# Kernel optimization log

Measured on AMD Instinct MI355X. Metric: run time of the kernel, lower is better.

Reference implementation:

```python
import jax, jax.numpy as jnp
import numpy as np

EPS = 1e-8


def _vb_layer(m, v, W_mu, W_var, relu_out, num_RF):
    """Variational linear layer with moment propagation.
    m: [N, in], v: [N, in] or None. W_mu/W_var: [out, in].
    """
    out_m = m @ W_mu.T
    m2 = m * m
    if v is None:
        out_v = m2 @ W_var.T
    else:
        out_v = (v + m2) @ W_var.T + v @ (W_mu * W_mu).T
    if relu_out:
        # random-feature ReLU output, scaled by sqrt(2/num_RF)
        scale = (2.0 / float(num_RF)) ** 0.5
        mask = (out_m > 0).astype(out_m.dtype)
        out_m = scale * jnp.maximum(out_m, 0.0)
        out_v = (scale * scale) * out_v * mask
    return out_m, out_v


def setup_inputs() -> dict:
    key = jax.random.key(0)
    ks = jax.random.split(key, 6)
    N, D0, R, D1, U = 262144, 128, 256, 64, 50000
    X = jax.random.normal(ks[0], (N, D0), dtype=jnp.float32)
    X_idx = jax.random.randint(ks[1], (N,), 0, U)
    W1_mu = jax.random.normal(ks[2], (R, D0), dtype=jnp.float32) / np.float32(np.sqrt(D0))
    W1_var = jax.random.uniform(ks[3], (R, D0), dtype=jnp.float32) * 0.1 + 0.01
    W2_mu = jax.random.normal(ks[4], (D1, R), dtype=jnp.float32) / np.float32(np.sqrt(R))
    W2_var = jax.random.uniform(ks[5], (D1, R), dtype=jnp.float32) * 0.1 + 0.01
    return {"X": X, "X_idx": X_idx, "W1_mu": W1_mu, "W1_var": W1_var,
            "W2_mu": W2_mu, "W2_var": W2_var, "num_unique": U}


def reference(X, X_idx, W1_mu, W1_var, W2_mu, W2_var, num_unique):
    num_RF = W1_mu.shape[0]
    # DGP layers: RF layer (ReLU features) then variational linear
    m, v = _vb_layer(X, None, W1_mu, W1_var, True, num_RF)
    m, v = _vb_layer(m, v, W2_mu, W2_var, False, num_RF)
    # precision-weighted segment reduction over X_idx
    precision = 1.0 / (v + EPS)          # [N, D1]
    weighted = precision * m             # [N, D1]
    p_sum = jax.ops.segment_sum(precision, X_idx, num_segments=num_unique) + EPS
    m_sum = jax.ops.segment_sum(weighted, X_idx, num_segments=num_unique)
    embedd_vars = 1.0 / p_sum            # [U, D1]
    embedd_means = m_sum * embedd_vars   # [U, D1]
    return embedd_means, embedd_vars
```

## Files before the change

kernel.cpp:

```cpp
#include <hip/hip_runtime.h>

#define EPSF 1e-8f

constexpr int D0 = 128;
constexpr int R  = 256;
constexpr int D1 = 64;
constexpr int BM = 64;
constexpr int NT = 512;
constexpr int TP = 68;

typedef __attribute__((ext_vector_type(8))) short  bf16x8;
typedef __attribute__((ext_vector_type(4))) float  f32x4;
typedef __attribute__((ext_vector_type(4))) uint   u32x4;

constexpr int WS_W1VAR = 32768;
constexpr int WS_W2MU  = 65536;
constexpr int WS_W2C   = 81920;
constexpr int WS_W2VAR = 98304;

__device__ __forceinline__ ushort f2bf(float x) {
    uint32_t u = __builtin_bit_cast(uint32_t, x);
    u += 0x7FFFu + ((u >> 16) & 1u);
    return (ushort)(u >> 16);
}

__device__ __forceinline__ uint cvt_pk_bf16(float lo, float hi) {
    uint r;
    asm("v_cvt_pk_bf16_f32 %0, %1, %2" : "=v"(r) : "v"(lo), "v"(hi));
    return r;
}

__device__ __forceinline__ bf16x8 sq_bf16x8(bf16x8 a) {
    u32x4 u = __builtin_bit_cast(u32x4, a);
    u32x4 r;
    #pragma unroll
    for (int i = 0; i < 4; ++i) {
        float lo = __builtin_bit_cast(float, u[i] << 16);
        float hi = __builtin_bit_cast(float, u[i] & 0xFFFF0000u);
        r[i] = cvt_pk_bf16(lo * lo, hi * hi);
    }
    return __builtin_bit_cast(bf16x8, r);
}

__global__ void convert_w(const float* __restrict__ W1mu,
                          const float* __restrict__ W1var,
                          const float* __restrict__ W2mu,
                          const float* __restrict__ W2var,
                          ushort* __restrict__ ws)
{
    int tid = blockIdx.x * 256 + threadIdx.x;
    if (tid < 8192) {
        int m    = tid >> 12;
        int f    = (tid >> 6) & 63;
        int lane = tid & 63;
        int nt = f >> 2, ks = f & 3;
        int col = nt * 16 + (lane & 15);
        int k0  = ks * 32 + (lane >> 4) * 8;
        const float* src = (m ? W1var : W1mu) + (size_t)col * D0 + k0;
        ushort* dst = ws + (m ? WS_W1VAR : 0) + (size_t)(f * 64 + lane) * 8;
        #pragma unroll
        for (int j = 0; j < 8; ++j) dst[j] = f2bf(src[j]);
    } else if (tid < 8192 + 3 * 2048) {
        int t2   = tid - 8192;
        int m    = t2 >> 11;
        int f    = (t2 >> 6) & 31;
        int lane = t2 & 63;
        int nt = f >> 3, ks = f & 7;
        int col = nt * 16 + (lane & 15);
        int k0  = ks * 32 + (lane >> 4) * 8;
        const float* smu = W2mu  + (size_t)col * R + k0;
        const float* svr = W2var + (size_t)col * R + k0;
        ushort* dst = ws + WS_W2MU + m * 16384 + (size_t)(f * 64 + lane) * 8;
        #pragma unroll
        for (int j = 0; j < 8; ++j) {
            float v;
            if (m == 0)      v = smu[j];
            else if (m == 1) v = fmaf(smu[j], smu[j], svr[j]);
            else             v = svr[j];
            dst[j] = f2bf(v);
        }
    }
}

__global__ __launch_bounds__(NT, 4)
void dgp_mfma(const float* __restrict__ X,
              const int*   __restrict__ Xidx,
              const ushort* __restrict__ ws,
              float* __restrict__ accM,
              float* __restrict__ accP)
{
    __shared__ __align__(16) ushort sh[2 * BM * R];
    ushort* M1s = sh;
    ushort* V1s = sh + BM * R;

    const int t    = threadIdx.x;
    const int lane = t & 63;
    const int w    = t >> 6;
    const int row0 = blockIdx.x * BM;
    const int lcol = lane & 15;
    const int lk   = lane >> 4;

    {
        float* Xs = (float*)sh;
        const float4* X4 = (const float4*)(X + (size_t)row0 * D0);
        #pragma unroll
        for (int i = 0; i < 4; ++i) {
            int g   = t + NT * i;
            int row = g >> 5, c4 = g & 31;
            float4 v = X4[g];
            int gran = c4 ^ (row & 7);
            *(float4*)&Xs[row * 128 + gran * 4] = v;
        }
    }
    __syncthreads();

    const float* Xs = (const float*)sh;
    f32x4 accm[2][4], accv[2][4];
    #pragma unroll
    for (int ntl = 0; ntl < 2; ++ntl)
        #pragma unroll
        for (int rt = 0; rt < 4; ++rt) {
            accm[ntl][rt] = (f32x4)0.f;
            accv[ntl][rt] = (f32x4)0.f;
        }

    #pragma unroll
    for (int ks = 0; ks < 4; ++ks) {
        bf16x8 amu[2], avr[2];
        #pragma unroll
        for (int ntl = 0; ntl < 2; ++ntl) {
            int f = (w * 2 + ntl) * 4 + ks;
            amu[ntl] = *(const bf16x8*)(ws + (size_t)(f * 64 + lane) * 8);
            avr[ntl] = *(const bf16x8*)(ws + WS_W1VAR + (size_t)(f * 64 + lane) * 8);
        }
        #pragma unroll
        for (int rt = 0; rt < 4; ++rt) {
            int xrow = rt * 16 + lcol;
            int g0 = (ks * 8 + lk * 2) ^ (xrow & 7);
            int g1 = (ks * 8 + lk * 2 + 1) ^ (xrow & 7);
            float4 a = *(const float4*)&Xs[xrow * 128 + g0 * 4];
            float4 b = *(const float4*)&Xs[xrow * 128 + g1 * 4];
            u32x4 um, uq;
            um[0] = cvt_pk_bf16(a.x, a.y);
            um[1] = cvt_pk_bf16(a.z, a.w);
            um[2] = cvt_pk_bf16(b.x, b.y);
            um[3] = cvt_pk_bf16(b.z, b.w);
            uq[0] = cvt_pk_bf16(a.x * a.x, a.y * a.y);
            uq[1] = cvt_pk_bf16(a.z * a.z, a.w * a.w);
            uq[2] = cvt_pk_bf16(b.x * b.x, b.y * b.y);
            uq[3] = cvt_pk_bf16(b.z * b.z, b.w * b.w);
            bf16x8 xb = __builtin_bit_cast(bf16x8, um);
            bf16x8 xq = __builtin_bit_cast(bf16x8, uq);
            #pragma unroll
            for (int ntl = 0; ntl < 2; ++ntl) {
                accm[ntl][rt] = __builtin_amdgcn_mfma_f32_16x16x32_bf16(amu[ntl], xb, accm[ntl][rt], 0, 0, 0);
                accv[ntl][rt] = __builtin_amdgcn_mfma_f32_16x16x32_bf16(avr[ntl], xq, accv[ntl][rt], 0, 0, 0);
            }
        }
    }

    __syncthreads();

    const float SCALE  = 0.08838834764831845f;
    const float SCALE2 = 0.0078125f;
    #pragma unroll
    for (int ntl = 0; ntl < 2; ++ntl) {
        int rf0 = (w * 2 + ntl) * 16 + lk * 4;
        #pragma unroll
        for (int rt = 0; rt < 4; ++rt) {
            int xrow = rt * 16 + lcol;
            float m1[4], v1[4];
            #pragma unroll
            for (int i = 0; i < 4; ++i) {
                float om = accm[ntl][rt][i];
                float ov = accv[ntl][rt][i];
                bool pos = om > 0.f;
                m1[i] = pos ? SCALE  * om : 0.f;
                v1[i] = pos ? SCALE2 * ov : 0.f;
            }
            uint2 pm, pv;
            pm.x = cvt_pk_bf16(m1[0], m1[1]); pm.y = cvt_pk_bf16(m1[2], m1[3]);
            pv.x = cvt_pk_bf16(v1[0], v1[1]); pv.y = cvt_pk_bf16(v1[2], v1[3]);
            int idx = xrow * 256 + (rf0 ^ ((xrow & 7) << 3));
            *(uint2*)&M1s[idx] = pm;
            *(uint2*)&V1s[idx] = pv;
        }
    }

    __syncthreads();

    const int d = w & 3;
    const int h = w >> 2;
    f32x4 m2a[4], v2a[4];
    #pragma unroll
    for (int rt = 0; rt < 4; ++rt) { m2a[rt] = (f32x4)0.f; v2a[rt] = (f32x4)0.f; }

    #pragma unroll
    for (int kk = 0; kk < 4; ++kk) {
        int ks = h * 4 + kk;
        int f  = d * 8 + ks;
        bf16x8 amu = *(const bf16x8*)(ws + WS_W2MU  + (size_t)(f * 64 + lane) * 8);
        bf16x8 ac  = *(const bf16x8*)(ws + WS_W2C   + (size_t)(f * 64 + lane) * 8);
        bf16x8 avr = *(const bf16x8*)(ws + WS_W2VAR + (size_t)(f * 64 + lane) * 8);
        #pragma unroll
        for (int rt = 0; rt < 4; ++rt) {
            int xrow = rt * 16 + lcol;
            int base = xrow * 256 + ((ks * 32 + lk * 8) ^ ((xrow & 7) << 3));
            bf16x8 bm  = *(const bf16x8*)&M1s[base];
            bf16x8 bv  = *(const bf16x8*)&V1s[base];
            bf16x8 bms = sq_bf16x8(bm);
            m2a[rt] = __builtin_amdgcn_mfma_f32_16x16x32_bf16(amu, bm,  m2a[rt], 0, 0, 0);
            v2a[rt] = __builtin_amdgcn_mfma_f32_16x16x32_bf16(ac,  bv,  v2a[rt], 0, 0, 0);
            v2a[rt] = __builtin_amdgcn_mfma_f32_16x16x32_bf16(avr, bms, v2a[rt], 0, 0, 0);
        }
    }

    __syncthreads();

    float* Vp = (float*)sh;
    float* Mp = Vp + BM * TP;
    if (h == 0) {
        #pragma unroll
        for (int rt = 0; rt < 4; ++rt) {
            int xrow = rt * 16 + lcol;
            int d1   = d * 16 + lk * 4;
            *(f32x4*)&Vp[xrow * TP + d1] = v2a[rt];
            *(f32x4*)&Mp[xrow * TP + d1] = m2a[rt];
        }
    }
    __syncthreads();
    if (h == 1) {
        #pragma unroll
        for (int rt = 0; rt < 4; ++rt) {
            int xrow = rt * 16 + lcol;
            int d1   = d * 16 + lk * 4;
            f32x4 vv = *(const f32x4*)&Vp[xrow * TP + d1];
            f32x4 mm = *(const f32x4*)&Mp[xrow * TP + d1];
            vv += v2a[rt];
            mm += m2a[rt];
            *(f32x4*)&Vp[xrow * TP + d1] = vv;
            *(f32x4*)&Mp[xrow * TP + d1] = mm;
        }
    }
    __syncthreads();

    #pragma unroll
    for (int r = 0; r < 8; ++r) {
        int row = w * 8 + r;
        int g   = __builtin_amdgcn_readfirstlane(Xidx[row0 + row]);
        float vv = Vp[row * TP + lane];
        float mm = Mp[row * TP + lane];
        float p  = 1.0f / (vv + EPSF);
        atomicAdd(accP + (size_t)g * D1 + lane, p);
        atomicAdd(accM + (size_t)g * D1 + lane, p * mm);
    }
}

__global__ void dgp_finalize(float* __restrict__ accM,
                             float* __restrict__ accP, int total)
{
    int idx = blockIdx.x * blockDim.x + threadIdx.x;
    if (idx < total) {
        float var = 1.0f / (accP[idx] + EPSF);
        accP[idx] = var;
        accM[idx] = accM[idx] * var;
    }
}

extern "C" void kernel_launch(void* const* d_in, const int* in_sizes, int n_in,
                              void* d_out, int out_size, void* d_ws, size_t ws_size,
                              hipStream_t stream)
{
    const float* X     = (const float*)d_in[0];
    const int*   Xidx  = (const int*)d_in[1];
    const float* W1mu  = (const float*)d_in[2];
    const float* W1var = (const float*)d_in[3];
    const float* W2mu  = (const float*)d_in[4];
    const float* W2var = (const float*)d_in[5];

    const int N = in_sizes[0] / D0;
    const int U = out_size / (2 * D1);
    float* out  = (float*)d_out;
    float* accM = out;
    float* accP = out + (size_t)U * D1;
    ushort* ws  = (ushort*)d_ws;

    hipMemsetAsync(d_out, 0, (size_t)out_size * sizeof(float), stream);

    convert_w<<<56, 256, 0, stream>>>(W1mu, W1var, W2mu, W2var, ws);

    dgp_mfma<<<N / BM, NT, 0, stream>>>(X, Xidx, ws, accM, accP);

    const int total = U * D1;
    dgp_finalize<<<(total + 255) / 256, 256, 0, stream>>>(accM, accP, total);
}
```

Before: 169.5 us.

## Pre-convert X to bf16 in LDS, fuse output zeroing, vectorize finalize

Each X tile is now converted once to bf16, along with its square, while staging into shared memory, instead of re-converting float data inside the MFMA k-loop for every use. The output memset is folded into the weight-conversion kernel, which now launches a larger grid, removing one launch. Division is replaced with the hardware reciprocal builtin, and the finalize kernel uses float4 accesses. The approximate reciprocal may change results slightly, and the float4 paths assume the output sizes are multiples of four.

```diff
diff --git a/kernel.cpp b/kernel.cpp
--- a/kernel.cpp
+++ b/kernel.cpp
@@ -30,6 +30,10 @@
     return r;
 }
 
+__device__ __forceinline__ float fastrcp(float x) {
+    return __builtin_amdgcn_rcpf(x);
+}
+
 __device__ __forceinline__ bf16x8 sq_bf16x8(bf16x8 a) {
     u32x4 u = __builtin_bit_cast(u32x4, a);
     u32x4 r;
@@ -46,7 +50,8 @@
                           const float* __restrict__ W1var,
                           const float* __restrict__ W2mu,
                           const float* __restrict__ W2var,
-                          ushort* __restrict__ ws)
+                          ushort* __restrict__ ws,
+                          float4* __restrict__ out4, int total4)
 {
     int tid = blockIdx.x * 256 + threadIdx.x;
     if (tid < 8192) {
@@ -80,6 +85,9 @@
             dst[j] = f2bf(v);
         }
     }
+    float4 z = {0.f, 0.f, 0.f, 0.f};
+    int nth = gridDim.x * 256;
+    for (int i = tid; i < total4; i += nth) out4[i] = z;
 }
 
 __global__ __launch_bounds__(NT, 4)
@@ -101,20 +109,36 @@
     const int lk   = lane >> 4;
 
     {
-        float* Xs = (float*)sh;
-        const float4* X4 = (const float4*)(X + (size_t)row0 * D0);
-        #pragma unroll
-        for (int i = 0; i < 4; ++i) {
-            int g   = t + NT * i;
-            int row = g >> 5, c4 = g & 31;
-            float4 v = X4[g];
-            int gran = c4 ^ (row & 7);
-            *(float4*)&Xs[row * 128 + gran * 4] = v;
-        }
-    }
-    __syncthreads();
-
-    const float* Xs = (const float*)sh;
+        ushort* XB = sh;
+        ushort* XQ = sh + 8192;
+        int row = t >> 3;
+        int cb  = t & 7;
+        const float4* src = (const float4*)(X + (size_t)(row0 + row) * D0) + cb * 4;
+        float4 a0 = src[0], a1 = src[1], a2 = src[2], a3 = src[3];
+        u32x4 b0, b1, q0, q1;
+        b0[0] = cvt_pk_bf16(a0.x, a0.y); b0[1] = cvt_pk_bf16(a0.z, a0.w);
+        b0[2] = cvt_pk_bf16(a1.x, a1.y); b0[3] = cvt_pk_bf16(a1.z, a1.w);
+        b1[0] = cvt_pk_bf16(a2.x, a2.y); b1[1] = cvt_pk_bf16(a2.z, a2.w);
+        b1[2] = cvt_pk_bf16(a3.x, a3.y); b1[3] = cvt_pk_bf16(a3.z, a3.w);
+        q0[0] = cvt_pk_bf16(a0.x * a0.x, a0.y * a0.y);
+        q0[1] = cvt_pk_bf16(a0.z * a0.z, a0.w * a0.w);
+        q0[2] = cvt_pk_bf16(a1.x * a1.x, a1.y * a1.y);
+        q0[3] = cvt_pk_bf16(a1.z * a1.z, a1.w * a1.w);
+        q1[0] = cvt_pk_bf16(a2.x * a2.x, a2.y * a2.y);
+        q1[1] = cvt_pk_bf16(a2.z * a2.z, a2.w * a2.w);
+        q1[2] = cvt_pk_bf16(a3.x * a3.x, a3.y * a3.y);
+        q1[3] = cvt_pk_bf16(a3.z * a3.z, a3.w * a3.w);
+        int gs0 = (cb * 2) ^ (row & 7);
+        int gs1 = (cb * 2 + 1) ^ (row & 7);
+        *(u32x4*)&XB[row * 128 + gs0 * 8] = b0;
+        *(u32x4*)&XB[row * 128 + gs1 * 8] = b1;
+        *(u32x4*)&XQ[row * 128 + gs0 * 8] = q0;
+        *(u32x4*)&XQ[row * 128 + gs1 * 8] = q1;
+    }
+    __syncthreads();
+
+    const ushort* XB = sh;
+    const ushort* XQ = sh + 8192;
     f32x4 accm[2][4], accv[2][4];
     #pragma unroll
     for (int ntl = 0; ntl < 2; ++ntl)
@@ -136,21 +160,9 @@
         #pragma unroll
         for (int rt = 0; rt < 4; ++rt) {
             int xrow = rt * 16 + lcol;
-            int g0 = (ks * 8 + lk * 2) ^ (xrow & 7);
-            int g1 = (ks * 8 + lk * 2 + 1) ^ (xrow & 7);
-            float4 a = *(const float4*)&Xs[xrow * 128 + g0 * 4];
-            float4 b = *(const float4*)&Xs[xrow * 128 + g1 * 4];
-            u32x4 um, uq;
-            um[0] = cvt_pk_bf16(a.x, a.y);
-            um[1] = cvt_pk_bf16(a.z, a.w);
-            um[2] = cvt_pk_bf16(b.x, b.y);
-            um[3] = cvt_pk_bf16(b.z, b.w);
-            uq[0] = cvt_pk_bf16(a.x * a.x, a.y * a.y);
-            uq[1] = cvt_pk_bf16(a.z * a.z, a.w * a.w);
-            uq[2] = cvt_pk_bf16(b.x * b.x, b.y * b.y);
-            uq[3] = cvt_pk_bf16(b.z * b.z, b.w * b.w);
-            bf16x8 xb = __builtin_bit_cast(bf16x8, um);
-            bf16x8 xq = __builtin_bit_cast(bf16x8, uq);
+            int gidx = (ks * 4 + lk) ^ (xrow & 7);
+            bf16x8 xb = *(const bf16x8*)&XB[xrow * 128 + gidx * 8];
+            bf16x8 xq = *(const bf16x8*)&XQ[xrow * 128 + gidx * 8];
             #pragma unroll
             for (int ntl = 0; ntl < 2; ++ntl) {
                 accm[ntl][rt] = __builtin_amdgcn_mfma_f32_16x16x32_bf16(amu[ntl], xb, accm[ntl][rt], 0, 0, 0);
@@ -250,20 +262,27 @@
         int g   = __builtin_amdgcn_readfirstlane(Xidx[row0 + row]);
         float vv = Vp[row * TP + lane];
         float mm = Mp[row * TP + lane];
-        float p  = 1.0f / (vv + EPSF);
+        float p  = fastrcp(vv + EPSF);
         atomicAdd(accP + (size_t)g * D1 + lane, p);
         atomicAdd(accM + (size_t)g * D1 + lane, p * mm);
     }
 }
 
-__global__ void dgp_finalize(float* __restrict__ accM,
-                             float* __restrict__ accP, int total)
+__global__ void dgp_finalize(float4* __restrict__ accM4,
+                             float4* __restrict__ accP4, int total4)
 {
     int idx = blockIdx.x * blockDim.x + threadIdx.x;
-    if (idx < total) {
-        float var = 1.0f / (accP[idx] + EPSF);
-        accP[idx] = var;
-        accM[idx] = accM[idx] * var;
+    if (idx < total4) {
+        float4 pv = accP4[idx];
+        float4 var;
+        var.x = fastrcp(pv.x + EPSF);
+        var.y = fastrcp(pv.y + EPSF);
+        var.z = fastrcp(pv.z + EPSF);
+        var.w = fastrcp(pv.w + EPSF);
+        accP4[idx] = var;
+        float4 mv = accM4[idx];
+        mv.x *= var.x; mv.y *= var.y; mv.z *= var.z; mv.w *= var.w;
+        accM4[idx] = mv;
     }
 }
 
@@ -284,13 +303,14 @@
     float* accM = out;
     float* accP = out + (size_t)U * D1;
     ushort* ws  = (ushort*)d_ws;
-
-    hipMemsetAsync(d_out, 0, (size_t)out_size * sizeof(float), stream);
-
-    convert_w<<<56, 256, 0, stream>>>(W1mu, W1var, W2mu, W2var, ws);
+    const int total4 = out_size / 4;
+
+    convert_w<<<2048, 256, 0, stream>>>(W1mu, W1var, W2mu, W2var, ws,
+                                        (float4*)d_out, total4);
 
     dgp_mfma<<<N / BM, NT, 0, stream>>>(X, Xidx, ws, accM, accP);
 
-    const int total = U * D1;
-    dgp_finalize<<<(total + 255) / 256, 256, 0, stream>>>(accM, accP, total);
-}
+    const int fin4 = (U * D1) / 4;
+    dgp_finalize<<<(fin4 + 255) / 256, 256, 0, stream>>>(
+        (float4*)accM, (float4*)accP, fin4);
+}
```

Result: faster. 159.1 us (-6.1%).
